# Optimization experiments

Measured on AMD Instinct MI355X. Metric: run time of the kernel, lower is better.

Reference implementation:

```python
import jax, jax.numpy as jnp
import numpy as np

CUTOFF = 3.5
EPS = 1e-7  # keras.backend.epsilon()


def triplet_indices(N):
    # All triplets (i, j, k) with j < k and j, k != i  -> [N, T, 3], T = (N-1)(N-2)/2
    idx = []
    for i in range(N):
        others = [a for a in range(N) if a != i]
        for a in range(len(others)):
            for b in range(a + 1, len(others)):
                idx.append((i, others[a], others[b]))
    T = (N - 1) * (N - 2) // 2
    return np.asarray(idx, dtype=np.int32).reshape(N, T, 3)


def f_C(distance):
    return 0.5 * jnp.cos(np.pi * distance / CUTOFF) + 0.5


def _he(key, shape):
    fan_in = shape[0]
    return jax.random.normal(key, shape, dtype=jnp.float32) * np.sqrt(2.0 / fan_in)


def setup_inputs() -> dict:
    key = jax.random.key(0)
    ks = jax.random.split(key, 10)
    B, N = 32, 32
    # build realistic symmetric distance matrices from random coordinates
    coords = jax.random.normal(ks[0], (B, N, 3), dtype=jnp.float32) * 2.0
    D = jnp.linalg.norm(coords[:, :, None, :] - coords[:, None, :, :], axis=-1)
    Z = jax.random.randint(ks[1], (B, N), 1, 10).astype(jnp.float32)
    dims = [(9, 64), (64, 64), (64, 64), (64, 64), (64, 64), (64, 128), (128, 256)]
    inp = {"distance_matrices": D, "num_species_batch": Z}
    for li, (fi, fo) in enumerate(dims):
        inp[f"W{li}"] = _he(ks[2 + li], (fi, fo))
        inp[f"b{li}"] = jnp.zeros((fo,), dtype=jnp.float32)
    return inp


def ang_mlp(x, W0, b0, W1, b1, W2, b2, W3, b3, W4, b4, W5, b5, W6, b6):
    x_res = jnp.tanh(x @ W0 + b0)
    h = jnp.tanh(x_res @ W1 + b1)
    blk1 = h + x_res
    h = jnp.tanh(blk1 @ W2 + b2)
    h = jnp.tanh(h @ W3 + b3)
    h = jnp.tanh(h @ W4 + b4)
    blk2 = h + blk1
    blk3 = jnp.tanh(blk2 @ W5 + b5)
    return jnp.tanh(blk3 @ W6 + b6)


def reference(distance_matrices, num_species_batch, W0, b0, W1, b1, W2, b2,
              W3, b3, W4, b4, W5, b5, W6, b6):
    D = distance_matrices          # [B, N, N]
    Z = num_species_batch          # [B, N]
    N = D.shape[1]
    trip = jnp.asarray(triplet_indices(N))          # [N, T, 3] static
    ti, tj, tk = trip[..., 0], trip[..., 1], trip[..., 2]   # each [N, T]

    # gather triplet distances / species -> [B, N, T]
    R_ij = D[:, ti, tj]
    R_ik = D[:, ti, tk]
    R_jk = D[:, tj, tk]
    z_i, z_j, z_k = Z[:, ti], Z[:, tj], Z[:, tk]

    # Carnot formula for angles
    def carnot(a, b, c):
        return (a ** 2 + b ** 2 - c ** 2) / jnp.maximum(2.0 * a * b, 1e-10)
    cos_i = carnot(R_ij, R_ik, R_jk)
    cos_j = carnot(R_ij, R_jk, R_ik)
    cos_k = carnot(R_ik, R_jk, R_ij)

    geo = jnp.stack([R_ij + R_ik + R_jk,
                     R_ij * R_ik + R_ij * R_jk + R_ik * R_jk,
                     R_ij * R_ik * R_jk], axis=-1)                      # [B,N,T,3]
    chem = jnp.stack([
        z_i + z_j + z_k,
        cos_i + cos_j + cos_k,
        z_i * (z_j + z_k) + z_j * z_k - cos_i * (cos_j + cos_k) - cos_j * cos_k,
        z_i * (cos_j + cos_k) + cos_i * (z_j + z_k) + z_j * cos_k + cos_j * z_k,
        z_i * (z_j * z_k - cos_j * cos_k) - cos_i * (z_j * cos_k + cos_j * z_k),
        z_i * (z_j * cos_k + cos_j * z_k) + cos_i * (z_j * z_k - cos_j * cos_k),
    ], axis=-1)                                                          # [B,N,T,6]
    geo = geo / (jnp.linalg.norm(geo, axis=-1, keepdims=True) + EPS)
    chem = chem / (jnp.linalg.norm(chem, axis=-1, keepdims=True) + EPS)
    mlp_in = jnp.concatenate([geo, chem], axis=-1)                       # [B,N,T,9]

    mlp_out = ang_mlp(mlp_in, W0, b0, W1, b1, W2, b2, W3, b3, W4, b4, W5, b5, W6, b6)  # [B,N,T,256]

    # cutoff smoothing; triplets with a central distance beyond the cutoff map to 0
    within = ((R_ij < CUTOFF) & (R_ik < CUTOFF)).astype(mlp_out.dtype)
    smooth = f_C(R_ij) * f_C(R_ik) * within                              # [B,N,T]
    aev = jnp.sum(mlp_out * smooth[..., None], axis=2)                   # [B,N,256]
    return aev
```

## Files before the change

kernel.cpp:

```cpp
#include <hip/hip_runtime.h>

namespace {

constexpr int T = 465;
constexpr float FCUT = 3.5f;
constexpr float PI_OVER_CUT = 0.8975979010256552f;
constexpr int REC = 12;
constexpr int K2_BLOCKS = 512;
constexpr int MAXROWS_HARD = 1024 * 480;

__device__ __forceinline__ float ftanh(float x) {
    x = fminf(fmaxf(x, -15.0f), 15.0f);
    const float e = __expf(2.0f * x);
    return (e - 1.0f) * __builtin_amdgcn_rcpf(e + 1.0f);
}

__device__ __forceinline__ float rl_f(float v, int l) {
    return __int_as_float(__builtin_amdgcn_readlane(__float_as_int(v), l));
}

__device__ __forceinline__ void unrank(int t, int i, int& j, int& k) {
    int a = (int)((61.0f - sqrtf(3721.0f - 8.0f * (float)t)) * 0.5f);
    a = a < 0 ? 0 : (a > 29 ? 29 : a);
    int rem = t - ((a * (61 - a)) >> 1);
    while (rem < 0) { --a; rem = t - ((a * (61 - a)) >> 1); }
    while (rem >= 30 - a) { rem -= 30 - a; ++a; }
    const int b = a + 1 + rem;
    j = a + (a >= i);
    k = b + (b >= i);
}

__global__ __launch_bounds__(256, 4)
void feat_kernel(const float* __restrict__ D, const float* __restrict__ Z,
                 float* __restrict__ rows, int* __restrict__ ctr, int maxrows)
{
    const int lane = threadIdx.x & 63;
    const int center = blockIdx.x * 4 + (threadIdx.x >> 6);
    const int bi = center >> 5, i = center & 31;
    const float* __restrict__ Drow = D + bi * 1024;
    const float* __restrict__ Zrow = Z + bi * 32;
    const float z_i = Zrow[i];

    unsigned long long masks[8];
    int cnt = 0;
    #pragma unroll
    for (int rnd = 0; rnd < 8; ++rnd) {
        const int t = rnd * 64 + lane;
        bool act = false;
        if (t < T) {
            int j, k;
            unrank(t, i, j, k);
            const float rij = Drow[i * 32 + j];
            const float rik = Drow[i * 32 + k];
            act = (rij < FCUT) && (rik < FCUT);
        }
        masks[rnd] = __ballot(act);
        cnt += (int)__popcll(masks[rnd]);
    }
    const int padded = (cnt + 15) & ~15;
    if (padded == 0) return;
    int base = 0;
    if (lane == 0) base = atomicAdd(ctr, padded);
    base = __shfl(base, 0);
    if (base + padded > maxrows) return;

    int pre = 0;
    #pragma unroll
    for (int rnd = 0; rnd < 8; ++rnd) {
        const unsigned long long mb = masks[rnd];
        const bool act = (mb >> lane) & 1ull;
        const int slot = base + pre + (int)__popcll(mb & ((1ull << lane) - 1ull));
        pre += (int)__popcll(mb);
        if (act) {
            const int t = rnd * 64 + lane;
            int j, k;
            unrank(t, i, j, k);
            const float rij = Drow[i * 32 + j];
            const float rik = Drow[i * 32 + k];
            const float rjk = Drow[j * 32 + k];
            const float zj = Zrow[j], zk = Zrow[k];
            const float rij2 = rij * rij, rik2 = rik * rik, rjk2 = rjk * rjk;
            const float ci = (rij2 + rik2 - rjk2) * __builtin_amdgcn_rcpf(fmaxf(2.f * rij * rik, 1e-10f));
            const float cj = (rij2 + rjk2 - rik2) * __builtin_amdgcn_rcpf(fmaxf(2.f * rij * rjk, 1e-10f));
            const float ck = (rik2 + rjk2 - rij2) * __builtin_amdgcn_rcpf(fmaxf(2.f * rik * rjk, 1e-10f));
            const float g0 = rij + rik + rjk;
            const float g1 = rij * rik + rij * rjk + rik * rjk;
            const float g2 = rij * rik * rjk;
            const float rg = __builtin_amdgcn_rcpf(sqrtf(g0 * g0 + g1 * g1 + g2 * g2) + 1e-7f);
            const float s0 = z_i + zj + zk;
            const float s1 = ci + cj + ck;
            const float s2 = z_i * (zj + zk) + zj * zk - ci * (cj + ck) - cj * ck;
            const float s3 = z_i * (cj + ck) + ci * (zj + zk) + zj * ck + cj * zk;
            const float s4 = z_i * (zj * zk - cj * ck) - ci * (zj * ck + cj * zk);
            const float s5 = z_i * (zj * ck + cj * zk) + ci * (zj * zk - cj * ck);
            const float rs = __builtin_amdgcn_rcpf(sqrtf(s0*s0 + s1*s1 + s2*s2 + s3*s3 + s4*s4 + s5*s5) + 1e-7f);
            const float fij = 0.5f * __cosf(PI_OVER_CUT * rij) + 0.5f;
            const float fik = 0.5f * __cosf(PI_OVER_CUT * rik) + 0.5f;
            float4* dst = (float4*)(rows + (size_t)slot * REC);
            dst[0] = make_float4(g0 * rg, g1 * rg, g2 * rg, s0 * rs);
            dst[1] = make_float4(s1 * rs, s2 * rs, s3 * rs, s4 * rs);
            dst[2] = make_float4(s5 * rs, fij * fik, __int_as_float(center), 0.f);
        }
    }
    for (int p = cnt + lane; p < padded; p += 64) {
        float4* dst = (float4*)(rows + (size_t)(base + p) * REC);
        dst[0] = make_float4(0.f, 0.f, 0.f, 0.f);
        dst[1] = make_float4(0.f, 0.f, 0.f, 0.f);
        dst[2] = make_float4(0.f, 0.f, __int_as_float(center), 0.f);
    }
}

template<int LDW>
__device__ __forceinline__ void accum64(const float* __restrict__ Wl,
                                        const float (&x)[16], float (&a)[16])
{
    #pragma unroll 1
    for (int kc = 0; kc < 8; ++kc) {
        float w[8];
        #pragma unroll
        for (int k = 0; k < 8; ++k) w[k] = Wl[(size_t)(kc * 8 + k) * LDW];
        const int kb = kc * 8;
        #pragma unroll
        for (int r = 0; r < 16; ++r) {
            #pragma unroll
            for (int k = 0; k < 8; ++k)
                a[r] = fmaf(rl_f(x[r], kb + k), w[k], a[r]);
        }
    }
}

template<int LDW>
__device__ __forceinline__ void accum64_pair(const float* __restrict__ Wl1,
                                             const float* __restrict__ Wl2,
                                             const float (&x)[16],
                                             float (&a1)[16], float (&a2)[16])
{
    #pragma unroll 1
    for (int kc = 0; kc < 8; ++kc) {
        float w1[8], w2[8];
        #pragma unroll
        for (int k = 0; k < 8; ++k) {
            w1[k] = Wl1[(size_t)(kc * 8 + k) * LDW];
            w2[k] = Wl2[(size_t)(kc * 8 + k) * LDW];
        }
        const int kb = kc * 8;
        #pragma unroll
        for (int r = 0; r < 16; ++r) {
            #pragma unroll
            for (int k = 0; k < 8; ++k) {
                const float s = rl_f(x[r], kb + k);
                a1[r] = fmaf(s, w1[k], a1[r]);
                a2[r] = fmaf(s, w2[k], a2[r]);
            }
        }
    }
}

__global__ __launch_bounds__(256, 2)
void mlp_kernel(const float* __restrict__ rows, const int* __restrict__ ctr,
                const float* __restrict__ W0, const float* __restrict__ B0,
                const float* __restrict__ W1, const float* __restrict__ B1,
                const float* __restrict__ W2, const float* __restrict__ B2,
                const float* __restrict__ W3, const float* __restrict__ B3,
                const float* __restrict__ W4, const float* __restrict__ B4,
                const float* __restrict__ W5, const float* __restrict__ B5,
                const float* __restrict__ W6, const float* __restrict__ B6,
                float* __restrict__ out, int maxrows)
{
    const int lane = threadIdx.x & 63;
    const int gw = blockIdx.x * 4 + (threadIdx.x >> 6);
    constexpr int TOTW = K2_BLOCKS * 4;

    int nrows = *ctr;
    if (nrows > maxrows) nrows = maxrows & ~15;
    const int nsegs = nrows >> 4;

    for (int s = gw; s < nsegs; s += TOTW) {
        float recv[16];
        const float* __restrict__ rp = rows + (size_t)s * 16 * REC;
        #pragma unroll
        for (int r = 0; r < 16; ++r)
            recv[r] = (lane < REC) ? rp[r * REC + lane] : 0.f;

        const int ct = __builtin_amdgcn_readlane(__float_as_int(recv[0]), 10);
        float smr[16];
        #pragma unroll
        for (int r = 0; r < 16; ++r) smr[r] = rl_f(recv[r], 9);

        float x[16], res[16];

        {
            float w0[9];
            #pragma unroll
            for (int k = 0; k < 9; ++k) w0[k] = W0[k * 64 + lane];
            const float b = B0[lane];
            #pragma unroll
            for (int r = 0; r < 16; ++r) {
                float a = b;
                #pragma unroll
                for (int k = 0; k < 9; ++k)
                    a = fmaf(rl_f(recv[r], k), w0[k], a);
                x[r] = ftanh(a);
            }
        }
        {
            float a[16]; const float b = B1[lane];
            #pragma unroll
            for (int r = 0; r < 16; ++r) a[r] = b;
            accum64<64>(W1 + lane, x, a);
            #pragma unroll
            for (int r = 0; r < 16; ++r) { x[r] = ftanh(a[r]) + x[r]; res[r] = x[r]; }
        }
        {
            float a[16]; const float b = B2[lane];
            #pragma unroll
            for (int r = 0; r < 16; ++r) a[r] = b;
            accum64<64>(W2 + lane, x, a);
            #pragma unroll
            for (int r = 0; r < 16; ++r) x[r] = ftanh(a[r]);
        }
        {
            float a[16]; const float b = B3[lane];
            #pragma unroll
            for (int r = 0; r < 16; ++r) a[r] = b;
            accum64<64>(W3 + lane, x, a);
            #pragma unroll
            for (int r = 0; r < 16; ++r) x[r] = ftanh(a[r]);
        }
        {
            float a[16]; const float b = B4[lane];
            #pragma unroll
            for (int r = 0; r < 16; ++r) a[r] = b;
            accum64<64>(W4 + lane, x, a);
            #pragma unroll
            for (int r = 0; r < 16; ++r) x[r] = ftanh(a[r]) + res[r];
        }
        float xA[16], xB[16];
        {
            float a[16]; const float b = B5[lane];
            #pragma unroll
            for (int r = 0; r < 16; ++r) a[r] = b;
            accum64<128>(W5 + lane, x, a);
            #pragma unroll
            for (int r = 0; r < 16; ++r) xA[r] = ftanh(a[r]);
        }
        {
            float a[16]; const float b = B5[64 + lane];
            #pragma unroll
            for (int r = 0; r < 16; ++r) a[r] = b;
            accum64<128>(W5 + 64 + lane, x, a);
            #pragma unroll
            for (int r = 0; r < 16; ++r) xB[r] = ftanh(a[r]);
        }
        #pragma unroll 1
        for (int p = 0; p < 2; ++p) {
            float a1[16], a2[16];
            const float b1 = B6[p * 128 + lane];
            const float b2 = B6[p * 128 + 64 + lane];
            #pragma unroll
            for (int r = 0; r < 16; ++r) { a1[r] = b1; a2[r] = b2; }
            accum64_pair<256>(W6 + p * 128 + lane,
                              W6 + p * 128 + 64 + lane, xA, a1, a2);
            accum64_pair<256>(W6 + 64 * 256 + p * 128 + lane,
                              W6 + 64 * 256 + p * 128 + 64 + lane, xB, a1, a2);
            float o1 = 0.f, o2 = 0.f;
            #pragma unroll
            for (int r = 0; r < 16; ++r) {
                o1 = fmaf(smr[r], ftanh(a1[r]), o1);
                o2 = fmaf(smr[r], ftanh(a2[r]), o2);
            }
            atomicAdd(out + (size_t)ct * 256 + p * 128 + lane, o1);
            atomicAdd(out + (size_t)ct * 256 + p * 128 + 64 + lane, o2);
        }
    }
}

}

extern "C" void kernel_launch(void* const* d_in, const int* in_sizes, int n_in,
                              void* d_out, int out_size, void* d_ws, size_t ws_size,
                              hipStream_t stream) {
    (void)in_sizes; (void)n_in;

    const float* D  = (const float*)d_in[0];
    const float* Z  = (const float*)d_in[1];
    const float* W0 = (const float*)d_in[2];  const float* B0 = (const float*)d_in[3];
    const float* W1 = (const float*)d_in[4];  const float* B1 = (const float*)d_in[5];
    const float* W2 = (const float*)d_in[6];  const float* B2 = (const float*)d_in[7];
    const float* W3 = (const float*)d_in[8];  const float* B3 = (const float*)d_in[9];
    const float* W4 = (const float*)d_in[10]; const float* B4 = (const float*)d_in[11];
    const float* W5 = (const float*)d_in[12]; const float* B5 = (const float*)d_in[13];
    const float* W6 = (const float*)d_in[14]; const float* B6 = (const float*)d_in[15];
    float* out = (float*)d_out;

    int* ctr = (int*)d_ws;
    float* rowbuf = (float*)((char*)d_ws + 64);
    size_t avail = (ws_size > 64) ? (ws_size - 64) / (REC * sizeof(float)) : 0;
    int maxrows = (int)((avail < (size_t)MAXROWS_HARD) ? avail : (size_t)MAXROWS_HARD);

    hipMemsetAsync(d_ws, 0, 64, stream);
    hipMemsetAsync(d_out, 0, sizeof(float) * (size_t)out_size, stream);

    feat_kernel<<<256, 256, 0, stream>>>(D, Z, rowbuf, ctr, maxrows);
    mlp_kernel<<<K2_BLOCKS, 256, 0, stream>>>(rowbuf, ctr,
                                              W0, B0, W1, B1, W2, B2, W3, B3,
                                              W4, B4, W5, B5, W6, B6, out, maxrows);
}
```

Baseline: 388.9 us.

## Map one row per lane with uniform scalar weight loads in MLP

Restructures the MLP kernel so that each lane owns one triplet row and all 64 output channels, instead of each lane owning one channel across 16 rows broadcast via readlane. Weights are read as wave-uniform 16-wide vectors through the constant address space, so they can go through scalar loads and feed FMAs as scalar operands. This removes the readlane broadcasts. The cost is very high register pressure (about 320 floats live per lane), with a real risk of spills and low occupancy. It also adds shuffle reductions over 16-lane groups, which assume rows sharing a center are 16-aligned, followed by 64 atomics per group.

```diff
diff --git a/kernel.cpp b/kernel.cpp
--- a/kernel.cpp
+++ b/kernel.cpp
@@ -6,17 +6,16 @@
 constexpr float FCUT = 3.5f;
 constexpr float PI_OVER_CUT = 0.8975979010256552f;
 constexpr int REC = 12;
-constexpr int K2_BLOCKS = 512;
+constexpr int K2_GRID = 1024;
 constexpr int MAXROWS_HARD = 1024 * 480;
+
+typedef float __attribute__((ext_vector_type(16))) f16v;
+typedef const __attribute__((address_space(4))) f16v* c16p;
 
 __device__ __forceinline__ float ftanh(float x) {
     x = fminf(fmaxf(x, -15.0f), 15.0f);
     const float e = __expf(2.0f * x);
     return (e - 1.0f) * __builtin_amdgcn_rcpf(e + 1.0f);
-}
-
-__device__ __forceinline__ float rl_f(float v, int l) {
-    return __int_as_float(__builtin_amdgcn_readlane(__float_as_int(v), l));
 }
 
 __device__ __forceinline__ void unrank(int t, int i, int& j, int& k) {
@@ -110,53 +109,35 @@
     }
 }
 
+__device__ __forceinline__ void bias64(const float* Bp, float (&acc)[64]) {
+    c16p bp = (c16p)(uintptr_t)Bp;
+    const f16v b0 = bp[0], b1 = bp[1], b2 = bp[2], b3 = bp[3];
+    #pragma unroll
+    for (int q = 0; q < 16; ++q) {
+        acc[q] = b0[q]; acc[16 + q] = b1[q]; acc[32 + q] = b2[q]; acc[48 + q] = b3[q];
+    }
+}
+
 template<int LDW>
-__device__ __forceinline__ void accum64(const float* __restrict__ Wl,
-                                        const float (&x)[16], float (&a)[16])
+__device__ __forceinline__ void layer64(const float* __restrict__ W,
+                                        const float* x, float (&acc)[64])
 {
-    #pragma unroll 1
-    for (int kc = 0; kc < 8; ++kc) {
-        float w[8];
-        #pragma unroll
-        for (int k = 0; k < 8; ++k) w[k] = Wl[(size_t)(kc * 8 + k) * LDW];
-        const int kb = kc * 8;
-        #pragma unroll
-        for (int r = 0; r < 16; ++r) {
-            #pragma unroll
-            for (int k = 0; k < 8; ++k)
-                a[r] = fmaf(rl_f(x[r], kb + k), w[k], a[r]);
-        }
-    }
-}
-
-template<int LDW>
-__device__ __forceinline__ void accum64_pair(const float* __restrict__ Wl1,
-                                             const float* __restrict__ Wl2,
-                                             const float (&x)[16],
-                                             float (&a1)[16], float (&a2)[16])
-{
-    #pragma unroll 1
-    for (int kc = 0; kc < 8; ++kc) {
-        float w1[8], w2[8];
-        #pragma unroll
-        for (int k = 0; k < 8; ++k) {
-            w1[k] = Wl1[(size_t)(kc * 8 + k) * LDW];
-            w2[k] = Wl2[(size_t)(kc * 8 + k) * LDW];
-        }
-        const int kb = kc * 8;
-        #pragma unroll
-        for (int r = 0; r < 16; ++r) {
-            #pragma unroll
-            for (int k = 0; k < 8; ++k) {
-                const float s = rl_f(x[r], kb + k);
-                a1[r] = fmaf(s, w1[k], a1[r]);
-                a2[r] = fmaf(s, w2[k], a2[r]);
-            }
-        }
-    }
-}
-
-__global__ __launch_bounds__(256, 2)
+    #pragma unroll 2
+    for (int k = 0; k < 64; ++k) {
+        c16p wp = (c16p)(uintptr_t)(W + (size_t)k * LDW);
+        const f16v w0 = wp[0], w1 = wp[1], w2 = wp[2], w3 = wp[3];
+        const float xv = x[k];
+        #pragma unroll
+        for (int q = 0; q < 16; ++q) {
+            acc[q]      = fmaf(xv, w0[q], acc[q]);
+            acc[16 + q] = fmaf(xv, w1[q], acc[16 + q]);
+            acc[32 + q] = fmaf(xv, w2[q], acc[32 + q]);
+            acc[48 + q] = fmaf(xv, w3[q], acc[48 + q]);
+        }
+    }
+}
+
+__global__ __launch_bounds__(64)
 void mlp_kernel(const float* __restrict__ rows, const int* __restrict__ ctr,
                 const float* __restrict__ W0, const float* __restrict__ B0,
                 const float* __restrict__ W1, const float* __restrict__ B1,
@@ -167,110 +148,96 @@
                 const float* __restrict__ W6, const float* __restrict__ B6,
                 float* __restrict__ out, int maxrows)
 {
-    const int lane = threadIdx.x & 63;
-    const int gw = blockIdx.x * 4 + (threadIdx.x >> 6);
-    constexpr int TOTW = K2_BLOCKS * 4;
-
+    const int lane = threadIdx.x;
     int nrows = *ctr;
     if (nrows > maxrows) nrows = maxrows & ~15;
-    const int nsegs = nrows >> 4;
-
-    for (int s = gw; s < nsegs; s += TOTW) {
-        float recv[16];
-        const float* __restrict__ rp = rows + (size_t)s * 16 * REC;
-        #pragma unroll
-        for (int r = 0; r < 16; ++r)
-            recv[r] = (lane < REC) ? rp[r * REC + lane] : 0.f;
-
-        const int ct = __builtin_amdgcn_readlane(__float_as_int(recv[0]), 10);
-        float smr[16];
-        #pragma unroll
-        for (int r = 0; r < 16; ++r) smr[r] = rl_f(recv[r], 9);
-
-        float x[16], res[16];
-
-        {
-            float w0[9];
+
+    for (int g = blockIdx.x; g * 64 < nrows; g += K2_GRID) {
+        const int row = g * 64 + lane;
+        float xin[9];
+        float sm = 0.f;
+        int ct = -1;
+        if (row < nrows) {
+            const float4* rp = (const float4*)(rows + (size_t)row * REC);
+            const float4 a = rp[0], b = rp[1], c = rp[2];
+            xin[0] = a.x; xin[1] = a.y; xin[2] = a.z; xin[3] = a.w;
+            xin[4] = b.x; xin[5] = b.y; xin[6] = b.z; xin[7] = b.w;
+            xin[8] = c.x; sm = c.y; ct = __float_as_int(c.z);
+        } else {
             #pragma unroll
-            for (int k = 0; k < 9; ++k) w0[k] = W0[k * 64 + lane];
-            const float b = B0[lane];
+            for (int q = 0; q < 9; ++q) xin[q] = 0.f;
+        }
+
+        float x[64], xA[64], xB[64];
+        float res[64], acc[64];
+
+        bias64(B0, acc);
+        #pragma unroll
+        for (int k = 0; k < 9; ++k) {
+            c16p wp = (c16p)(uintptr_t)(W0 + k * 64);
+            const f16v w0 = wp[0], w1 = wp[1], w2 = wp[2], w3 = wp[3];
+            const float xv = xin[k];
             #pragma unroll
-            for (int r = 0; r < 16; ++r) {
-                float a = b;
+            for (int q = 0; q < 16; ++q) {
+                acc[q]      = fmaf(xv, w0[q], acc[q]);
+                acc[16 + q] = fmaf(xv, w1[q], acc[16 + q]);
+                acc[32 + q] = fmaf(xv, w2[q], acc[32 + q]);
+                acc[48 + q] = fmaf(xv, w3[q], acc[48 + q]);
+            }
+        }
+        #pragma unroll
+        for (int c = 0; c < 64; ++c) { const float v = ftanh(acc[c]); x[c] = v; res[c] = v; }
+
+        bias64(B1, acc);
+        layer64<64>(W1, x, acc);
+        #pragma unroll
+        for (int c = 0; c < 64; ++c) { const float v = ftanh(acc[c]) + res[c]; x[c] = v; res[c] = v; }
+
+        bias64(B2, acc);
+        layer64<64>(W2, x, acc);
+        #pragma unroll
+        for (int c = 0; c < 64; ++c) x[c] = ftanh(acc[c]);
+
+        bias64(B3, acc);
+        layer64<64>(W3, x, acc);
+        #pragma unroll
+        for (int c = 0; c < 64; ++c) x[c] = ftanh(acc[c]);
+
+        bias64(B4, acc);
+        layer64<64>(W4, x, acc);
+        #pragma unroll
+        for (int c = 0; c < 64; ++c) x[c] = ftanh(acc[c]) + res[c];
+
+        bias64(B5, acc);
+        layer64<128>(W5, x, acc);
+        #pragma unroll
+        for (int c = 0; c < 64; ++c) xA[c] = ftanh(acc[c]);
+
+        bias64(B5 + 64, acc);
+        layer64<128>(W5 + 64, x, acc);
+        #pragma unroll
+        for (int c = 0; c < 64; ++c) xB[c] = ftanh(acc[c]);
+
+        #pragma unroll 1
+        for (int ch = 0; ch < 4; ++ch) {
+            const int c0 = ch * 64;
+            bias64(B6 + c0, acc);
+            layer64<256>(W6 + c0, xA, acc);
+            layer64<256>(W6 + 64 * 256 + c0, xB, acc);
+            #pragma unroll
+            for (int c = 0; c < 64; ++c) {
+                float v = ftanh(acc[c]) * sm;
+                v += __shfl_xor(v, 1);
+                v += __shfl_xor(v, 2);
+                v += __shfl_xor(v, 4);
+                v += __shfl_xor(v, 8);
+                acc[c] = v;
+            }
+            if (((lane & 15) == 0) && ct >= 0) {
+                float* __restrict__ op = out + (size_t)ct * 256 + c0;
                 #pragma unroll
-                for (int k = 0; k < 9; ++k)
-                    a = fmaf(rl_f(recv[r], k), w0[k], a);
-                x[r] = ftanh(a);
+                for (int c = 0; c < 64; ++c) atomicAdd(op + c, acc[c]);
             }
-        }
-        {
-            float a[16]; const float b = B1[lane];
-            #pragma unroll
-            for (int r = 0; r < 16; ++r) a[r] = b;
-            accum64<64>(W1 + lane, x, a);
-            #pragma unroll
-            for (int r = 0; r < 16; ++r) { x[r] = ftanh(a[r]) + x[r]; res[r] = x[r]; }
-        }
-        {
-            float a[16]; const float b = B2[lane];
-            #pragma unroll
-            for (int r = 0; r < 16; ++r) a[r] = b;
-            accum64<64>(W2 + lane, x, a);
-            #pragma unroll
-            for (int r = 0; r < 16; ++r) x[r] = ftanh(a[r]);
-        }
-        {
-            float a[16]; const float b = B3[lane];
-            #pragma unroll
-            for (int r = 0; r < 16; ++r) a[r] = b;
-            accum64<64>(W3 + lane, x, a);
-            #pragma unroll
-            for (int r = 0; r < 16; ++r) x[r] = ftanh(a[r]);
-        }
-        {
-            float a[16]; const float b = B4[lane];
-            #pragma unroll
-            for (int r = 0; r < 16; ++r) a[r] = b;
-            accum64<64>(W4 + lane, x, a);
-            #pragma unroll
-            for (int r = 0; r < 16; ++r) x[r] = ftanh(a[r]) + res[r];
-        }
-        float xA[16], xB[16];
-        {
-            float a[16]; const float b = B5[lane];
-            #pragma unroll
-            for (int r = 0; r < 16; ++r) a[r] = b;
-            accum64<128>(W5 + lane, x, a);
-            #pragma unroll
-            for (int r = 0; r < 16; ++r) xA[r] = ftanh(a[r]);
-        }
-        {
-            float a[16]; const float b = B5[64 + lane];
-            #pragma unroll
-            for (int r = 0; r < 16; ++r) a[r] = b;
-            accum64<128>(W5 + 64 + lane, x, a);
-            #pragma unroll
-            for (int r = 0; r < 16; ++r) xB[r] = ftanh(a[r]);
-        }
-        #pragma unroll 1
-        for (int p = 0; p < 2; ++p) {
-            float a1[16], a2[16];
-            const float b1 = B6[p * 128 + lane];
-            const float b2 = B6[p * 128 + 64 + lane];
-            #pragma unroll
-            for (int r = 0; r < 16; ++r) { a1[r] = b1; a2[r] = b2; }
-            accum64_pair<256>(W6 + p * 128 + lane,
-                              W6 + p * 128 + 64 + lane, xA, a1, a2);
-            accum64_pair<256>(W6 + 64 * 256 + p * 128 + lane,
-                              W6 + 64 * 256 + p * 128 + 64 + lane, xB, a1, a2);
-            float o1 = 0.f, o2 = 0.f;
-            #pragma unroll
-            for (int r = 0; r < 16; ++r) {
-                o1 = fmaf(smr[r], ftanh(a1[r]), o1);
-                o2 = fmaf(smr[r], ftanh(a2[r]), o2);
-            }
-            atomicAdd(out + (size_t)ct * 256 + p * 128 + lane, o1);
-            atomicAdd(out + (size_t)ct * 256 + p * 128 + 64 + lane, o2);
         }
     }
 }
@@ -302,7 +269,7 @@
     hipMemsetAsync(d_out, 0, sizeof(float) * (size_t)out_size, stream);
 
     feat_kernel<<<256, 256, 0, stream>>>(D, Z, rowbuf, ctr, maxrows);
-    mlp_kernel<<<K2_BLOCKS, 256, 0, stream>>>(rowbuf, ctr,
-                                              W0, B0, W1, B1, W2, B2, W3, B3,
-                                              W4, B4, W5, B5, W6, B6, out, maxrows);
-}
+    mlp_kernel<<<K2_GRID, 64, 0, stream>>>(rowbuf, ctr,
+                                           W0, B0, W1, B1, W2, B2, W3, B3,
+                                           W4, B4, W5, B5, W6, B6, out, maxrows);
+}
```

Result: slower. 1.168 ms (+200.3%).
